# Optimization experiments

Hardware: AMD Instinct MI355X
Metric: run time of the kernel (lower is better)

The kernel has to match this reference:

```python
import jax, jax.numpy as jnp
import numpy as np

T, D, DFF = 8192, 512, 2048
EPS = 1e-5
LS_INIT = 1e-4

def setup_inputs() -> dict:
    key = jax.random.key(0)
    ks = jax.random.split(key, 5)
    s = 0.02
    return {
        "x": jax.random.normal(ks[0], (T, D), jnp.float32),
        "W_in": jax.random.normal(ks[1], (3 * D, D), jnp.float32) * s,
        "W_out": jax.random.normal(ks[2], (D, D), jnp.float32) * s,
        "W1": jax.random.normal(ks[3], (DFF, D), jnp.float32) * s,
        "W2": jax.random.normal(ks[4], (D, DFF), jnp.float32) * s,
        "g1": jnp.ones((D,), jnp.float32),
        "b1": jnp.zeros((D,), jnp.float32),
        "g2": jnp.ones((D,), jnp.float32),
        "b2": jnp.zeros((D,), jnp.float32),
        "ls1": jnp.full((D,), LS_INIT, jnp.float32),
        "ls2": jnp.full((D,), LS_INIT, jnp.float32),
    }

def _layer_norm(x, g, b):
    mu = jnp.mean(x, axis=-1, keepdims=True)
    var = jnp.mean((x - mu) ** 2, axis=-1, keepdims=True)
    return (x - mu) * jax.lax.rsqrt(var + EPS) * g + b

def reference(x, W_in, W_out, W1, W2, g1, b1, g2, b2, ls1, ls2):
    t = x.shape[0]
    # --- self-attention block (faithful: no head split, no 1/sqrt(d) scale, k @ q^T) ---
    h = _layer_norm(x, g1, b1)                       # [T, D]
    proj = h @ W_in.T                                # [T, 3D]
    q, k, v = jnp.split(proj, 3, axis=-1)            # each [T, D]
    scores = k @ q.T                                 # [T, T]
    mask = jnp.tril(jnp.ones((t, t), scores.dtype))
    scores = jnp.where(mask == 0, -jnp.inf, scores)
    attn = jax.nn.softmax(scores, axis=-1)
    o = (attn @ v) @ W_out.T                         # [T, D]
    x = x + ls1 * o
    # --- FFN block ---
    h = _layer_norm(x, g2, b2)
    update = jax.nn.gelu(h @ W1.T) @ W2.T            # [T, D]
    return x + ls2 * update
```

## Files before the change

kernel.cpp:

```cpp
#include <hip/hip_runtime.h>
#include <hip/hip_bf16.h>


using bf16 = __hip_bfloat16;
typedef __attribute__((ext_vector_type(8))) short short8;
typedef __attribute__((ext_vector_type(4))) short short4v;
typedef __attribute__((ext_vector_type(4))) float f32x4;

#define T_DIM 8192

#define AS1C(p) (const __attribute__((address_space(1))) void*)(p)
#define AS3P(p) (__attribute__((address_space(3))) void*)(p)
#define GLL16(src, dst) __builtin_amdgcn_global_load_lds(AS1C(src), AS3P(dst), 16, 0, 0)

static __device__ __forceinline__ short f2bfbits(float f) {
  bf16 b = __float2bfloat16(f);
  short s; __builtin_memcpy(&s, &b, 2); return s;
}
static __device__ __forceinline__ float bfbits2f(short s) {
  unsigned u = ((unsigned)(unsigned short)s) << 16;
  float f; __builtin_memcpy(&f, &u, 4); return f;
}

__global__ void cvt4_kernel(
    const float* __restrict__ a, bf16* __restrict__ oa, int na,
    const float* __restrict__ b, bf16* __restrict__ ob, int nb,
    const float* __restrict__ c, bf16* __restrict__ oc, int nc,
    const float* __restrict__ d, bf16* __restrict__ od, int nd)
{
  int i = blockIdx.x * 256 + threadIdx.x;
  const float* src; bf16* dst;
  if (i < na / 4) { src = a; dst = oa; }
  else { i -= na / 4;
    if (i < nb / 4) { src = b; dst = ob; }
    else { i -= nb / 4;
      if (i < nc / 4) { src = c; dst = oc; }
      else { i -= nc / 4;
        if (i >= nd / 4) return;
        src = d; dst = od; } } }
  const f32x4 v = ((const f32x4*)src)[i];
  short4v o;
#pragma unroll
  for (int j = 0; j < 4; ++j) o[j] = f2bfbits(v[j]);
  ((short4v*)dst)[i] = o;
}

__global__ __launch_bounds__(256) void ln_kernel(
    const float* __restrict__ x, const float* __restrict__ g,
    const float* __restrict__ bb, bf16* __restrict__ h)
{
  const int row = blockIdx.x * 4 + (threadIdx.x >> 6);
  const int lane = threadIdx.x & 63;
  const float* xr = x + (size_t)row * 512 + lane * 8;
  f32x4 v0 = *(const f32x4*)xr;
  f32x4 v1 = *(const f32x4*)(xr + 4);
  float s = 0.f;
#pragma unroll
  for (int j = 0; j < 4; ++j) s += v0[j] + v1[j];
#pragma unroll
  for (int d = 1; d < 64; d <<= 1) s += __shfl_xor(s, d);
  const float mu = s * (1.f / 512.f);
  float vs = 0.f;
#pragma unroll
  for (int j = 0; j < 4; ++j) { float a = v0[j] - mu, b2 = v1[j] - mu; vs += a * a + b2 * b2; }
#pragma unroll
  for (int d = 1; d < 64; d <<= 1) vs += __shfl_xor(vs, d);
  const float rs = rsqrtf(vs * (1.f / 512.f) + 1e-5f);
  const f32x4 g0 = *(const f32x4*)(g + lane * 8);
  const f32x4 g1v = *(const f32x4*)(g + lane * 8 + 4);
  const f32x4 b0 = *(const f32x4*)(bb + lane * 8);
  const f32x4 b1v = *(const f32x4*)(bb + lane * 8 + 4);
  short8 ov;
#pragma unroll
  for (int j = 0; j < 4; ++j) {
    ov[j]     = f2bfbits((v0[j] - mu) * rs * g0[j] + b0[j]);
    ov[j + 4] = f2bfbits((v1[j] - mu) * rs * g1v[j] + b1v[j]);
  }
  *(short8*)(h + (size_t)row * 512 + lane * 8) = ov;
}

enum { MODE_BF16 = 0, MODE_GELU = 1, MODE_RESID = 2 };

static __device__ __forceinline__ float gelu_f(float x) {
  float x3 = x * x * x;
  float t = tanhf(0.7978845608028654f * (x + 0.044715f * x3));
  return 0.5f * x * (1.0f + t);
}

template <int MODE>
__global__ __launch_bounds__(256, 2) void gemm_bt(
    const bf16* __restrict__ A, const bf16* __restrict__ B,
    int M, int N, int K,
    bf16* __restrict__ Cb, float* __restrict__ Cf,
    const float* __restrict__ resid, const float* __restrict__ scale)
{
  __shared__ bf16 sA[128 * 64];
  __shared__ bf16 sB[128 * 64];
  const int tid = threadIdx.x;
  const int lane = tid & 63, wave = tid >> 6;
  const int NB = gridDim.y;
  const int nwg = gridDim.x * NB;
  const int lin = blockIdx.y * gridDim.x + blockIdx.x;
  const int q8 = nwg >> 3;
  const int swz = (lin & 7) * q8 + (lin >> 3);
  const int bm = swz / NB, bn = swz % NB;
  const int wm = (wave & 1) * 64, wn = (wave >> 1) * 64;
  const int ln = lane & 15, lg = lane >> 4;
  f32x4 acc[4][4] = {};

  const int nkt = K >> 6;
  for (int kt = 0; kt < nkt; ++kt) {
    __syncthreads();
#pragma unroll
    for (int r = 0; r < 4; ++r) {
      const int s = r * 256 + tid;
      const int ks = s >> 9, rb = (s >> 6) & 7, l = s & 63;
      const bf16* srcA = A + (size_t)(bm * 128 + rb * 16 + (l & 15)) * K + kt * 64 + ks * 32 + (l >> 4) * 8;
      GLL16(srcA, sA + (size_t)(r * 256 + wave * 64) * 8);
      const bf16* srcB = B + (size_t)(bn * 128 + rb * 16 + (l & 15)) * K + kt * 64 + ks * 32 + (l >> 4) * 8;
      GLL16(srcB, sB + (size_t)(r * 256 + wave * 64) * 8);
    }
    __syncthreads();
#pragma unroll
    for (int ks = 0; ks < 2; ++ks) {
      short8 af[4], bfr[4];
#pragma unroll
      for (int mi = 0; mi < 4; ++mi)
        af[mi] = *(const short8*)(sA + (size_t)(ks * 512 + ((wm >> 4) + mi) * 64 + lane) * 8);
#pragma unroll
      for (int ni = 0; ni < 4; ++ni)
        bfr[ni] = *(const short8*)(sB + (size_t)(ks * 512 + ((wn >> 4) + ni) * 64 + lane) * 8);
#pragma unroll
      for (int mi = 0; mi < 4; ++mi)
#pragma unroll
        for (int ni = 0; ni < 4; ++ni)
          acc[mi][ni] = __builtin_amdgcn_mfma_f32_16x16x32_bf16(af[mi], bfr[ni], acc[mi][ni], 0, 0, 0);
    }
  }
#pragma unroll
  for (int mi = 0; mi < 4; ++mi) {
#pragma unroll
    for (int ni = 0; ni < 4; ++ni) {
#pragma unroll
      for (int r = 0; r < 4; ++r) {
        const int row = bm * 128 + wm + mi * 16 + lg * 4 + r;
        const int col = bn * 128 + wn + ni * 16 + ln;
        const size_t idx = (size_t)row * N + col;
        float v = acc[mi][ni][r];
        if constexpr (MODE == MODE_GELU) { Cb[idx] = __float2bfloat16(gelu_f(v)); }
        else if constexpr (MODE == MODE_RESID) { Cf[idx] = resid[idx] + scale[col] * v; }
        else { Cb[idx] = __float2bfloat16(v); }
      }
    }
  }
}

__global__ __launch_bounds__(256) void transpose_v(const bf16* __restrict__ proj, bf16* __restrict__ vT) {
  __shared__ bf16 tile[64][66];
  const int t0 = blockIdx.x * 64, d0 = blockIdx.y * 64;
  const int tid = threadIdx.x;
#pragma unroll
  for (int i = 0; i < 16; ++i) {
    const int lin = i * 256 + tid;
    const int r = lin >> 6, c = lin & 63;
    tile[r][c] = proj[(size_t)(t0 + r) * 1536 + 1024 + d0 + c];
  }
  __syncthreads();
#pragma unroll
  for (int i = 0; i < 16; ++i) {
    const int lin = i * 256 + tid;
    const int dy = lin >> 6, tx = lin & 63;
    vT[(size_t)(d0 + dy) * T_DIM + t0 + tx] = tile[tx][dy];
  }
}

__global__ __launch_bounds__(512, 2) void attn_kernel(
    const bf16* __restrict__ proj, const bf16* __restrict__ vT,
    bf16* __restrict__ Op, float* __restrict__ mlp)
{
  __shared__ bf16 sQ[2][32 * 512];
  __shared__ bf16 sV[2][32 * 512];
  __shared__ bf16 sP[8][16 * 40];

  const int tid = threadIdx.x, lane = tid & 63, wave = tid >> 6;
  const int ln = lane & 15, lg = lane >> 4;
  const int b = 511 - blockIdx.x;
  const int it = b >> 3;
  const int ch = b & 7;
  const int nj = 4 * it + 4;
  const int jlo = ch * nj / 8;
  const int jhi = (ch + 1) * nj / 8;
  const int wrow = it * 128 + wave * 16;

  short8 kf[16];
#pragma unroll
  for (int ks = 0; ks < 16; ++ks)
    kf[ks] = *(const short8*)(proj + (size_t)(wrow + ln) * 1536 + 512 + ks * 32 + lg * 8);

  f32x4 oa[32] = {};
  float m_r[4] = {-__builtin_inff(), -__builtin_inff(), -__builtin_inff(), -__builtin_inff()};
  float l_r[4] = {0.f, 0.f, 0.f, 0.f};

  auto stageQ = [&](int c, int jt) {
    const int j0 = jt * 32;
#pragma unroll
    for (int r = 0; r < 4; ++r) {
      const int s = r * 512 + tid;
      const int l = s & 63;
      const int ks = s >> 7, jb = (s >> 6) & 1;
      const bf16* srcQ = proj + (size_t)(j0 + jb * 16 + (l & 15)) * 1536 + ks * 32 + (l >> 4) * 8;
      GLL16(srcQ, &sQ[c][(size_t)(r * 512 + wave * 64) * 8]);
    }
  };
  auto stageV = [&](int c, int jt) {
    const int j0 = jt * 32;
#pragma unroll
    for (int r = 0; r < 4; ++r) {
      const int s = r * 512 + tid;
      const int l = s & 63;
      const int nb = s >> 6;
      const bf16* srcV = vT + (size_t)(nb * 16 + (l & 15)) * T_DIM + j0 + (l >> 4) * 8;
      GLL16(srcV, &sV[c][(size_t)(r * 512 + wave * 64) * 8]);
    }
  };

  if (jlo < jhi) {
    int cur = 0;
    stageQ(0, jlo);
    stageV(0, jlo);
    for (int jt = jlo; jt < jhi; ++jt) {
      const int j0 = jt * 32;
      const bool more = (jt + 1 < jhi);
      if (more) stageQ(cur ^ 1, jt + 1);
      if (more) { asm volatile("s_waitcnt vmcnt(8)" ::: "memory"); }
      else      { asm volatile("s_waitcnt vmcnt(4)" ::: "memory"); }
      __builtin_amdgcn_s_barrier();
      __builtin_amdgcn_sched_barrier(0);
      if (j0 <= wrow + 15) {
        f32x4 sfr[2] = {};
        __builtin_amdgcn_s_setprio(1);
#pragma unroll
        for (int ks = 0; ks < 16; ++ks) {
          short8 q0 = *(const short8*)(&sQ[cur][(size_t)(ks * 128 + lane) * 8]);
          short8 q1 = *(const short8*)(&sQ[cur][(size_t)(ks * 128 + 64 + lane) * 8]);
          sfr[0] = __builtin_amdgcn_mfma_f32_16x16x32_bf16(kf[ks], q0, sfr[0], 0, 0, 0);
          sfr[1] = __builtin_amdgcn_mfma_f32_16x16x32_bf16(kf[ks], q1, sfr[1], 0, 0, 0);
        }
        __builtin_amdgcn_s_setprio(0);
        if (j0 + 31 > wrow) {
#pragma unroll
          for (int jb = 0; jb < 2; ++jb)
#pragma unroll
            for (int r = 0; r < 4; ++r) {
              const int i = wrow + lg * 4 + r, j = j0 + jb * 16 + ln;
              if (j > i) sfr[jb][r] = -__builtin_inff();
            }
        }
        float mx[4];
#pragma unroll
        for (int r = 0; r < 4; ++r) mx[r] = fmaxf(sfr[0][r], sfr[1][r]);
#pragma unroll
        for (int d = 1; d < 16; d <<= 1)
#pragma unroll
          for (int r = 0; r < 4; ++r) mx[r] = fmaxf(mx[r], __shfl_xor(mx[r], d));
        bool need = false;
#pragma unroll
        for (int r = 0; r < 4; ++r) need |= !(mx[r] - m_r[r] <= 8.0f);
        if (__any(need)) {
          float sc[4];
#pragma unroll
          for (int r = 0; r < 4; ++r) {
            float mm = fmaxf(fmaxf(m_r[r], mx[r]), -1e30f);
            sc[r] = __expf(m_r[r] - mm);
            m_r[r] = mm;
            l_r[r] *= sc[r];
          }
#pragma unroll
          for (int nb = 0; nb < 32; ++nb)
#pragma unroll
            for (int r = 0; r < 4; ++r) oa[nb][r] *= sc[r];
        }
        float ts[4] = {0.f, 0.f, 0.f, 0.f};
#pragma unroll
        for (int jb = 0; jb < 2; ++jb)
#pragma unroll
          for (int r = 0; r < 4; ++r) {
            float p = __expf(sfr[jb][r] - m_r[r]);
            sfr[jb][r] = p;
            ts[r] += p;
          }
#pragma unroll
        for (int d = 1; d < 16; d <<= 1)
#pragma unroll
          for (int r = 0; r < 4; ++r) ts[r] += __shfl_xor(ts[r], d);
#pragma unroll
        for (int r = 0; r < 4; ++r) l_r[r] += ts[r];
#pragma unroll
        for (int jb = 0; jb < 2; ++jb)
#pragma unroll
          for (int r = 0; r < 4; ++r)
            sP[wave][(lg * 4 + r) * 40 + jb * 16 + ln] = __float2bfloat16(sfr[jb][r]);
      }
      if (more) stageV(cur ^ 1, jt + 1);
      if (more) { asm volatile("s_waitcnt vmcnt(8)" ::: "memory"); }
      else      { asm volatile("s_waitcnt vmcnt(0)" ::: "memory"); }
      __builtin_amdgcn_s_barrier();
      __builtin_amdgcn_sched_barrier(0);
      if (j0 <= wrow + 15) {
        const short8 pa = *(const short8*)(&sP[wave][0] + ln * 40 + lg * 8);
        __builtin_amdgcn_s_setprio(1);
#define LDV(nb) (*(const short8*)(&sV[cur][(size_t)((nb) * 64 + lane) * 8]))
        short8 vf0 = LDV(0), vf1 = LDV(1), vf2 = LDV(2), vf3 = LDV(3);
#pragma unroll
        for (int nb = 0; nb < 28; nb += 4) {
          const short8 w0 = vf0, w1 = vf1, w2 = vf2, w3 = vf3;
          vf0 = LDV(nb + 4); vf1 = LDV(nb + 5); vf2 = LDV(nb + 6); vf3 = LDV(nb + 7);
          oa[nb]     = __builtin_amdgcn_mfma_f32_16x16x32_bf16(pa, w0, oa[nb],     0, 0, 0);
          oa[nb + 1] = __builtin_amdgcn_mfma_f32_16x16x32_bf16(pa, w1, oa[nb + 1], 0, 0, 0);
          oa[nb + 2] = __builtin_amdgcn_mfma_f32_16x16x32_bf16(pa, w2, oa[nb + 2], 0, 0, 0);
          oa[nb + 3] = __builtin_amdgcn_mfma_f32_16x16x32_bf16(pa, w3, oa[nb + 3], 0, 0, 0);
        }
        oa[28] = __builtin_amdgcn_mfma_f32_16x16x32_bf16(pa, vf0, oa[28], 0, 0, 0);
        oa[29] = __builtin_amdgcn_mfma_f32_16x16x32_bf16(pa, vf1, oa[29], 0, 0, 0);
        oa[30] = __builtin_amdgcn_mfma_f32_16x16x32_bf16(pa, vf2, oa[30], 0, 0, 0);
        oa[31] = __builtin_amdgcn_mfma_f32_16x16x32_bf16(pa, vf3, oa[31], 0, 0, 0);
#undef LDV
        __builtin_amdgcn_s_setprio(0);
      }
      cur ^= 1;
    }
  }
#pragma unroll
  for (int nb = 0; nb < 32; ++nb)
#pragma unroll
    for (int r = 0; r < 4; ++r)
      Op[((size_t)ch * T_DIM + wrow + lg * 4 + r) * 512 + nb * 16 + ln] = __float2bfloat16(oa[nb][r]);
  if (ln == 0) {
#pragma unroll
    for (int r = 0; r < 4; ++r) {
      mlp[((size_t)ch * T_DIM + wrow + lg * 4 + r) * 2 + 0] = m_r[r];
      mlp[((size_t)ch * T_DIM + wrow + lg * 4 + r) * 2 + 1] = l_r[r];
    }
  }
}

__global__ __launch_bounds__(256) void combine_kernel(
    const bf16* __restrict__ Op, const float* __restrict__ mlp, bf16* __restrict__ o)
{
  const int row = blockIdx.x * 4 + (threadIdx.x >> 6);
  const int lane = threadIdx.x & 63;
  const int k = 8;
  float m = -__builtin_inff();
  for (int c = 0; c < k; ++c) m = fmaxf(m, mlp[((size_t)c * T_DIM + row) * 2]);
  float l = 0.f;
  for (int c = 0; c < k; ++c) {
    const float mc = mlp[((size_t)c * T_DIM + row) * 2];
    const float lc = mlp[((size_t)c * T_DIM + row) * 2 + 1];
    l += __expf(mc - m) * lc;
  }
  const float inv = 1.0f / l;
  f32x4 a0 = {}, a1 = {};
  for (int c = 0; c < k; ++c) {
    const float w = __expf(mlp[((size_t)c * T_DIM + row) * 2] - m);
    const short8 u = *(const short8*)(Op + ((size_t)c * T_DIM + row) * 512 + lane * 8);
#pragma unroll
    for (int j = 0; j < 4; ++j) {
      a0[j] += w * bfbits2f(u[j]);
      a1[j] += w * bfbits2f(u[j + 4]);
    }
  }
  short8 ov;
#pragma unroll
  for (int j = 0; j < 4; ++j) {
    ov[j]     = f2bfbits(a0[j] * inv);
    ov[j + 4] = f2bfbits(a1[j] * inv);
  }
  *(short8*)(o + (size_t)row * 512 + lane * 8) = ov;
}

extern "C" void kernel_launch(void* const* d_in, const int* in_sizes, int n_in,
                              void* d_out, int out_size, void* d_ws, size_t ws_size,
                              hipStream_t stream) {
  (void)in_sizes; (void)n_in; (void)out_size; (void)ws_size;
  const float* x    = (const float*)d_in[0];
  const float* Win  = (const float*)d_in[1];
  const float* Wout = (const float*)d_in[2];
  const float* W1   = (const float*)d_in[3];
  const float* W2   = (const float*)d_in[4];
  const float* g1   = (const float*)d_in[5];
  const float* b1   = (const float*)d_in[6];
  const float* g2   = (const float*)d_in[7];
  const float* b2   = (const float*)d_in[8];
  const float* ls1  = (const float*)d_in[9];
  const float* ls2  = (const float*)d_in[10];
  float* out = (float*)d_out;

  char* w = (char*)d_ws;
  size_t off = 0;
  auto alloc = [&](size_t bytes) -> char* {
    char* p = w + off; off += (bytes + 255) & ~(size_t)255; return p;
  };
  bf16* wWin  = (bf16*)alloc((size_t)1536 * 512 * 2);
  bf16* wWout = (bf16*)alloc((size_t)512 * 512 * 2);
  bf16* wW1   = (bf16*)alloc((size_t)2048 * 512 * 2);
  bf16* wW2   = (bf16*)alloc((size_t)512 * 2048 * 2);
  bf16* h     = (bf16*)alloc((size_t)T_DIM * 512 * 2);
  bf16* proj  = (bf16*)alloc((size_t)T_DIM * 1536 * 2);
  bf16* vTb   = (bf16*)alloc((size_t)512 * T_DIM * 2);
  bf16* o     = (bf16*)alloc((size_t)T_DIM * 512 * 2);
  float* x1   = (float*)alloc((size_t)T_DIM * 512 * 4);
  bf16* Op    = (bf16*)alloc((size_t)8 * T_DIM * 512 * 2);
  float* mlp  = (float*)alloc((size_t)8 * T_DIM * 2 * 4);
  bf16* f1 = proj;

  cvt4_kernel<<<(1536 * 512 + 512 * 512 + 2048 * 512 + 512 * 2048) / 4 / 256, 256, 0, stream>>>(
      Win, wWin, 1536 * 512, Wout, wWout, 512 * 512,
      W1, wW1, 2048 * 512, W2, wW2, 512 * 2048);

  ln_kernel<<<T_DIM / 4, 256, 0, stream>>>(x, g1, b1, h);
  gemm_bt<MODE_BF16><<<dim3(64, 12), 256, 0, stream>>>(h, wWin, 8192, 1536, 512, proj, nullptr, nullptr, nullptr);
  transpose_v<<<dim3(T_DIM / 64, 8), 256, 0, stream>>>(proj, vTb);
  attn_kernel<<<512, 512, 0, stream>>>(proj, vTb, Op, mlp);
  combine_kernel<<<T_DIM / 4, 256, 0, stream>>>(Op, mlp, o);
  gemm_bt<MODE_RESID><<<dim3(64, 4), 256, 0, stream>>>(o, wWout, 8192, 512, 512, nullptr, x1, x, ls1);
  ln_kernel<<<T_DIM / 4, 256, 0, stream>>>(x1, g2, b2, h);
  gemm_bt<MODE_GELU><<<dim3(64, 16), 256, 0, stream>>>(h, wW1, 8192, 2048, 512, f1, nullptr, nullptr, nullptr);
  gemm_bt<MODE_RESID><<<dim3(64, 4), 256, 0, stream>>>(f1, wW2, 8192, 512, 2048, nullptr, out, x1, ls2);
}
```

Before: 320.3 us.

## Split-K the output projections and stage GEMM epilogue through LDS for coalesced stores

The two N=512 GEMMs (W_out and W2) now use split-K over blockIdx.z (2 and 4 splits), so the grid grows from 256 to 512 or 1024 workgroups. Partial results are written as bf16 and summed by a new resid_combine kernel that also applies the layer-scale residual. The GEMM epilogue now writes its tile into shared memory and stores rows as 16-byte vectors instead of scattered scalar stores. The cost is extra partial-sum traffic, a second kernel launch per GEMM, and bf16 rounding of the partials before they are summed.

```diff
diff --git a/kernel.cpp b/kernel.cpp
--- a/kernel.cpp
+++ b/kernel.cpp
@@ -79,7 +79,7 @@
   *(short8*)(h + (size_t)row * 512 + lane * 8) = ov;
 }
 
-enum { MODE_BF16 = 0, MODE_GELU = 1, MODE_RESID = 2 };
+enum { MODE_BF16 = 0, MODE_GELU = 1 };
 
 static __device__ __forceinline__ float gelu_f(float x) {
   float x3 = x * x * x;
@@ -90,12 +90,12 @@
 template <int MODE>
 __global__ __launch_bounds__(256, 2) void gemm_bt(
     const bf16* __restrict__ A, const bf16* __restrict__ B,
-    int M, int N, int K,
-    bf16* __restrict__ Cb, float* __restrict__ Cf,
-    const float* __restrict__ resid, const float* __restrict__ scale)
-{
-  __shared__ bf16 sA[128 * 64];
-  __shared__ bf16 sB[128 * 64];
+    int M, int N, int K, int ld,
+    bf16* __restrict__ Cb)
+{
+  __shared__ bf16 sS[128 * 136];
+  bf16* sA = sS;
+  bf16* sB = sS + 8192;
   const int tid = threadIdx.x;
   const int lane = tid & 63, wave = tid >> 6;
   const int NB = gridDim.y;
@@ -104,6 +104,8 @@
   const int q8 = nwg >> 3;
   const int swz = (lin & 7) * q8 + (lin >> 3);
   const int bm = swz / NB, bn = swz % NB;
+  const int z = blockIdx.z;
+  const int koff = z * K;
   const int wm = (wave & 1) * 64, wn = (wave >> 1) * 64;
   const int ln = lane & 15, lg = lane >> 4;
   f32x4 acc[4][4] = {};
@@ -115,9 +117,9 @@
     for (int r = 0; r < 4; ++r) {
       const int s = r * 256 + tid;
       const int ks = s >> 9, rb = (s >> 6) & 7, l = s & 63;
-      const bf16* srcA = A + (size_t)(bm * 128 + rb * 16 + (l & 15)) * K + kt * 64 + ks * 32 + (l >> 4) * 8;
+      const bf16* srcA = A + (size_t)(bm * 128 + rb * 16 + (l & 15)) * ld + koff + kt * 64 + ks * 32 + (l >> 4) * 8;
       GLL16(srcA, sA + (size_t)(r * 256 + wave * 64) * 8);
-      const bf16* srcB = B + (size_t)(bn * 128 + rb * 16 + (l & 15)) * K + kt * 64 + ks * 32 + (l >> 4) * 8;
+      const bf16* srcB = B + (size_t)(bn * 128 + rb * 16 + (l & 15)) * ld + koff + kt * 64 + ks * 32 + (l >> 4) * 8;
       GLL16(srcB, sB + (size_t)(r * 256 + wave * 64) * 8);
     }
     __syncthreads();
@@ -137,22 +139,55 @@
           acc[mi][ni] = __builtin_amdgcn_mfma_f32_16x16x32_bf16(af[mi], bfr[ni], acc[mi][ni], 0, 0, 0);
     }
   }
-#pragma unroll
-  for (int mi = 0; mi < 4; ++mi) {
-#pragma unroll
-    for (int ni = 0; ni < 4; ++ni) {
+  __syncthreads();
+#pragma unroll
+  for (int mi = 0; mi < 4; ++mi)
+#pragma unroll
+    for (int ni = 0; ni < 4; ++ni)
 #pragma unroll
       for (int r = 0; r < 4; ++r) {
-        const int row = bm * 128 + wm + mi * 16 + lg * 4 + r;
-        const int col = bn * 128 + wn + ni * 16 + ln;
-        const size_t idx = (size_t)row * N + col;
         float v = acc[mi][ni][r];
-        if constexpr (MODE == MODE_GELU) { Cb[idx] = __float2bfloat16(gelu_f(v)); }
-        else if constexpr (MODE == MODE_RESID) { Cf[idx] = resid[idx] + scale[col] * v; }
-        else { Cb[idx] = __float2bfloat16(v); }
+        if constexpr (MODE == MODE_GELU) v = gelu_f(v);
+        sS[(size_t)(wm + mi * 16 + lg * 4 + r) * 136 + wn + ni * 16 + ln] = __float2bfloat16(v);
       }
-    }
-  }
+  __syncthreads();
+  const int orow = tid >> 1, oc0 = (tid & 1) * 64;
+#pragma unroll
+  for (int v = 0; v < 8; ++v)
+    *(short8*)(Cb + ((size_t)z * M + bm * 128 + orow) * N + bn * 128 + oc0 + v * 8) =
+        *(const short8*)(sS + (size_t)orow * 136 + oc0 + v * 8);
+}
+
+__global__ __launch_bounds__(256) void resid_combine(
+    const bf16* __restrict__ Opc, int nc,
+    const float* __restrict__ resid, const float* __restrict__ scale,
+    float* __restrict__ outp)
+{
+  const int row = blockIdx.x * 4 + (threadIdx.x >> 6);
+  const int lane = threadIdx.x & 63;
+  f32x4 a0 = {}, a1 = {};
+  for (int c = 0; c < nc; ++c) {
+    const short8 u = *(const short8*)(Opc + ((size_t)c * T_DIM + row) * 512 + lane * 8);
+#pragma unroll
+    for (int j = 0; j < 4; ++j) {
+      a0[j] += bfbits2f(u[j]);
+      a1[j] += bfbits2f(u[j + 4]);
+    }
+  }
+  const float* rp = resid + (size_t)row * 512 + lane * 8;
+  const f32x4 r0 = *(const f32x4*)rp;
+  const f32x4 r1 = *(const f32x4*)(rp + 4);
+  const f32x4 s0 = *(const f32x4*)(scale + lane * 8);
+  const f32x4 s1 = *(const f32x4*)(scale + lane * 8 + 4);
+  f32x4 o0, o1;
+#pragma unroll
+  for (int j = 0; j < 4; ++j) {
+    o0[j] = r0[j] + s0[j] * a0[j];
+    o1[j] = r1[j] + s1[j] * a1[j];
+  }
+  float* op = outp + (size_t)row * 512 + lane * 8;
+  *(f32x4*)op = o0;
+  *(f32x4*)(op + 4) = o1;
 }
 
 __global__ __launch_bounds__(256) void transpose_v(const bf16* __restrict__ proj, bf16* __restrict__ vT) {
@@ -411,19 +446,23 @@
   float* x1   = (float*)alloc((size_t)T_DIM * 512 * 4);
   bf16* Op    = (bf16*)alloc((size_t)8 * T_DIM * 512 * 2);
   float* mlp  = (float*)alloc((size_t)8 * T_DIM * 2 * 4);
-  bf16* f1 = proj;
+  bf16* f1  = proj;
+  bf16* Opw = Op;
+  bf16* Opf = Op + (size_t)2 * T_DIM * 512;
 
   cvt4_kernel<<<(1536 * 512 + 512 * 512 + 2048 * 512 + 512 * 2048) / 4 / 256, 256, 0, stream>>>(
       Win, wWin, 1536 * 512, Wout, wWout, 512 * 512,
       W1, wW1, 2048 * 512, W2, wW2, 512 * 2048);
 
   ln_kernel<<<T_DIM / 4, 256, 0, stream>>>(x, g1, b1, h);
-  gemm_bt<MODE_BF16><<<dim3(64, 12), 256, 0, stream>>>(h, wWin, 8192, 1536, 512, proj, nullptr, nullptr, nullptr);
+  gemm_bt<MODE_BF16><<<dim3(64, 12, 1), 256, 0, stream>>>(h, wWin, 8192, 1536, 512, 512, proj);
   transpose_v<<<dim3(T_DIM / 64, 8), 256, 0, stream>>>(proj, vTb);
   attn_kernel<<<512, 512, 0, stream>>>(proj, vTb, Op, mlp);
   combine_kernel<<<T_DIM / 4, 256, 0, stream>>>(Op, mlp, o);
-  gemm_bt<MODE_RESID><<<dim3(64, 4), 256, 0, stream>>>(o, wWout, 8192, 512, 512, nullptr, x1, x, ls1);
+  gemm_bt<MODE_BF16><<<dim3(64, 4, 2), 256, 0, stream>>>(o, wWout, 8192, 512, 256, 512, Opw);
+  resid_combine<<<T_DIM / 4, 256, 0, stream>>>(Opw, 2, x, ls1, x1);
   ln_kernel<<<T_DIM / 4, 256, 0, stream>>>(x1, g2, b2, h);
-  gemm_bt<MODE_GELU><<<dim3(64, 16), 256, 0, stream>>>(h, wW1, 8192, 2048, 512, f1, nullptr, nullptr, nullptr);
-  gemm_bt<MODE_RESID><<<dim3(64, 4), 256, 0, stream>>>(f1, wW2, 8192, 512, 2048, nullptr, out, x1, ls2);
-}
+  gemm_bt<MODE_GELU><<<dim3(64, 16, 1), 256, 0, stream>>>(h, wW1, 8192, 2048, 512, 512, f1);
+  gemm_bt<MODE_BF16><<<dim3(64, 4, 4), 256, 0, stream>>>(f1, wW2, 8192, 512, 512, 2048, Opf);
+  resid_combine<<<T_DIM / 4, 256, 0, stream>>>(Opf, 4, x1, ls2, out);
+}
```

After: 344.5 us. 7.6% more time.
